# Performance work log

Measured on AMD Instinct MI355X. Metric: run time of the kernel, lower is better.

The kernel has to match this reference:

```python
import jax, jax.numpy as jnp
import numpy as np

BLOCK_SIZE = 256
N_EMBD = 256
HEAD_SIZE = 64


def setup_inputs() -> dict:
    key = jax.random.key(0)
    k1, k2, k3, k4, k5 = jax.random.split(key, 5)
    B, T = 256, 256
    x = jax.random.normal(k1, (B, T, N_EMBD), dtype=jnp.float32)
    # nn.Linear(n_embd, head_size, bias=False) weights, stored as [in, out] for x @ W
    s = 1.0 / np.sqrt(N_EMBD)
    Wk = jax.random.uniform(k2, (N_EMBD, HEAD_SIZE), minval=-s, maxval=s, dtype=jnp.float32)
    Wq = jax.random.uniform(k3, (N_EMBD, HEAD_SIZE), minval=-s, maxval=s, dtype=jnp.float32)
    Wv = jax.random.uniform(k4, (N_EMBD, HEAD_SIZE), minval=-s, maxval=s, dtype=jnp.float32)
    rel_pos_embedding = 0.02 * jax.random.normal(k5, (2 * BLOCK_SIZE - 1, HEAD_SIZE), dtype=jnp.float32)
    return {"x": x, "Wk": Wk, "Wq": Wq, "Wv": Wv, "rel_pos_embedding": rel_pos_embedding}


def reference(x, Wk, Wq, Wv, rel_pos_embedding):
    B, T, C = x.shape
    H = Wk.shape[-1]
    k = x @ Wk  # [B,T,H]
    q = x @ Wq  # [B,T,H]
    v = x @ Wv  # [B,T,H]
    # content scores (scaled); note: position scores are NOT scaled, matching original
    content = jnp.einsum('bth,bsh->bts', q, k) * (H ** -0.5)  # [B,T,T]
    # relative position indices: j - i + (block_size - 1)
    idx = jnp.arange(T)[None, :] - jnp.arange(T)[:, None] + (BLOCK_SIZE - 1)  # [T,T]
    rel_emb = rel_pos_embedding[idx]  # [T,T,H]
    position = jnp.einsum('bth,tsh->bts', q, rel_emb)  # [B,T,T]
    wei = content + position
    causal = jnp.tril(jnp.ones((T, T), dtype=bool))
    wei = jnp.where(causal[None, :, :], wei, -jnp.inf)
    wei = jax.nn.softmax(wei, axis=-1)
    # dropout omitted (eval mode / deterministic reference)
    out = jnp.einsum('bts,bsh->bth', wei, v)  # [B,T,H]
    return out
```

## Files before the change

kernel.cpp:

```cpp
#include <hip/hip_runtime.h>

#define BB 256
#define TT 256
#define CC 256
#define HH 64

typedef _Float16 half8 __attribute__((ext_vector_type(8)));
typedef _Float16 half4 __attribute__((ext_vector_type(4)));
typedef __fp16 fp16x2 __attribute__((ext_vector_type(2)));
typedef float floatx4 __attribute__((ext_vector_type(4)));

__global__ __launch_bounds__(256) void prep(
    const float* __restrict__ rpe,
    const float* __restrict__ Wk, const float* __restrict__ Wq, const float* __restrict__ Wv,
    _Float16* __restrict__ rpeh, _Float16* __restrict__ WT)
{
    const int bid = blockIdx.x, tid = threadIdx.x;
    if (bid < 64) {
        const int i = bid * 256 + tid;
        rpeh[i] = (_Float16)rpe[i];
    } else {
        const int wsel = (bid - 64) >> 6;
        const int n    = (bid - 64) & 63;
        const float* W = wsel == 0 ? Wk : (wsel == 1 ? Wq : Wv);
        WT[(size_t)(wsel * 64 + n) * 256 + tid] = (_Float16)W[tid * HH + n];
    }
}

__global__ __launch_bounds__(1024) void proj_mfma(
    const float* __restrict__ x, const _Float16* __restrict__ WT,
    _Float16* __restrict__ qh, _Float16* __restrict__ kh, _Float16* __restrict__ vTh)
{
    __shared__ _Float16 ws[192 * 256];
    const int tid = threadIdx.x;

#pragma unroll
    for (int i = tid; i < 192 * 32; i += 1024) {
        const int row = i >> 5;
        const int g   = i & 31;
        const int pg  = g ^ (row & 31);
        *(half8*)&ws[row * 256 + pg * 8] = *(const half8*)(WT + (size_t)row * 256 + g * 8);
    }
    __syncthreads();

    const int w    = tid >> 6;
    const int lane = tid & 63;
    const int quad = lane >> 4;
    const int l    = lane & 15;
    const int row0 = blockIdx.x * 256 + w * 16;

    floatx4 acc[12];
#pragma unroll
    for (int nt = 0; nt < 12; ++nt) acc[nt] = (floatx4){0.f, 0.f, 0.f, 0.f};

    const float4* xg = reinterpret_cast<const float4*>(x);
    union H8 { half8 v; fp16x2 p[4]; };

#pragma unroll
    for (int kk = 0; kk < 8; ++kk) {
        const size_t base = (size_t)(row0 + l) * 64 + kk * 8 + quad * 2;
        const float4 alo = xg[base], ahi = xg[base + 1];
        H8 u;
        u.p[0] = __builtin_amdgcn_cvt_pkrtz(alo.x, alo.y);
        u.p[1] = __builtin_amdgcn_cvt_pkrtz(alo.z, alo.w);
        u.p[2] = __builtin_amdgcn_cvt_pkrtz(ahi.x, ahi.y);
        u.p[3] = __builtin_amdgcn_cvt_pkrtz(ahi.z, ahi.w);

#pragma unroll
        for (int nt = 0; nt < 12; ++nt) {
            const int row = nt * 16 + l;
            const int pg  = (kk * 4 + quad) ^ (row & 31);
            const half8 bf = *(const half8*)&ws[row * 256 + pg * 8];
            acc[nt] = __builtin_amdgcn_mfma_f32_16x16x32_f16(u.v, bf, acc[nt], 0, 0, 0);
        }
    }

    const int bq  = blockIdx.x;
    const int trw = w * 16;
#pragma unroll
    for (int nt = 0; nt < 4; ++nt) {
#pragma unroll
        for (int r = 0; r < 4; ++r) {
            const size_t row = (size_t)row0 + quad * 4 + r;
            kh[row * HH + nt * 16 + l] = (_Float16)(acc[nt][r] * 0.125f);
            qh[row * HH + nt * 16 + l] = (_Float16)acc[nt + 4][r];
        }
        half4 vv;
        vv[0] = (_Float16)acc[nt + 8][0];
        vv[1] = (_Float16)acc[nt + 8][1];
        vv[2] = (_Float16)acc[nt + 8][2];
        vv[3] = (_Float16)acc[nt + 8][3];
        *(half4*)(vTh + ((size_t)bq * HH + nt * 16 + l) * TT + trw + quad * 4) = vv;
    }
}

__global__ __launch_bounds__(256) void flash(
    const _Float16* __restrict__ qh, const _Float16* __restrict__ kh,
    const _Float16* __restrict__ vTh, const _Float16* __restrict__ rpeh,
    float* __restrict__ out)
{
    __shared__ _Float16 weih[4][16 * 264];

    const int xcd  = blockIdx.x & 7;
    const int j    = blockIdx.x >> 3;
    const int b    = xcd * 32 + (j & 31);
    const int t0   = (j >> 5) * 64;
    const int w    = threadIdx.x >> 6;
    const int lane = threadIdx.x & 63;
    const int quad = lane >> 4;
    const int l    = lane & 15;
    const int tw   = t0 + 16 * w;
    const int stmax = tw >> 4;
    const int cmax  = (tw + 15) >> 5;
    const int dtmin = 15 - stmax;

    const _Float16* qp = qh + (size_t)(b * TT + tw + l) * HH + quad * 8;
    const half8 qf0 = *(const half8*)qp;
    const half8 qf1 = *(const half8*)(qp + 32);

#pragma unroll
    for (int dt = 0; dt < 16; ++dt) {
        if (dt >= dtmin) {
            const _Float16* rp = rpeh + (size_t)(dt * 16 + l) * HH + quad * 8;
            const half8 bf0 = *(const half8*)rp;
            const half8 bf1 = *(const half8*)(rp + 32);
            floatx4 z = {0.f, 0.f, 0.f, 0.f};
            z = __builtin_amdgcn_mfma_f32_16x16x32_f16(qf0, bf0, z, 0, 0, 0);
            const floatx4 pacc = __builtin_amdgcn_mfma_f32_16x16x32_f16(qf1, bf1, z, 0, 0, 0);
            if (dt == dtmin) {
#pragma unroll
                for (int r = 0; r < 4; ++r) {
                    const int row = quad * 4 + r;
                    const int s   = l + row - 15;
                    if (s >= 0) weih[w][row * 264 + s] = (_Float16)pacc[r];
                }
            } else {
#pragma unroll
                for (int r = 0; r < 4; ++r) {
                    const int row = quad * 4 + r;
                    const int s   = dt * 16 + l + tw + row - 255;
                    weih[w][row * 264 + s] = (_Float16)pacc[r];
                }
            }
        }
    }

    floatx4 sacc[16];
#pragma unroll
    for (int st = 0; st < 16; ++st) {
        if (st <= stmax) {
            const _Float16* kp = kh + (size_t)(b * TT + st * 16 + l) * HH + quad * 8;
            const half8 kf0 = *(const half8*)kp;
            const half8 kf1 = *(const half8*)(kp + 32);
            floatx4 z = {0.f, 0.f, 0.f, 0.f};
            z = __builtin_amdgcn_mfma_f32_16x16x32_f16(qf0, kf0, z, 0, 0, 0);
            sacc[st] = __builtin_amdgcn_mfma_f32_16x16x32_f16(qf1, kf1, z, 0, 0, 0);
        }
    }

    float sums[4] = {0.f, 0.f, 0.f, 0.f};
#pragma unroll
    for (int st = 0; st < 16; ++st) {
        if (st < stmax) {
            const int s = l + 16 * st;
#pragma unroll
            for (int r = 0; r < 4; ++r) {
                const int row = quad * 4 + r;
                const float e = __expf(sacc[st][r] + (float)weih[w][row * 264 + s]);
                sums[r] += e;
                weih[w][row * 264 + s] = (_Float16)e;
            }
        }
    }
    {
        const int s = l + 16 * stmax;
#pragma unroll
        for (int r = 0; r < 4; ++r) {
            const int row = quad * 4 + r;
            float e = 0.f;
            if (l <= row) e = __expf(sacc[stmax][r] + (float)weih[w][row * 264 + s]);
            sums[r] += e;
            weih[w][row * 264 + s] = (_Float16)e;
        }
    }
    if ((tw & 16) == 0) {
        const int s = l + 16 * (stmax + 1);
#pragma unroll
        for (int r = 0; r < 4; ++r) weih[w][(quad * 4 + r) * 264 + s] = (_Float16)0.f;
    }

    float inv_r[4];
#pragma unroll
    for (int r = 0; r < 4; ++r) {
        float sum = sums[r];
        sum += __shfl_xor(sum, 1);
        sum += __shfl_xor(sum, 2);
        sum += __shfl_xor(sum, 4);
        sum += __shfl_xor(sum, 8);
        inv_r[r] = 1.0f / sum;
    }

    floatx4 oacc[4] = {{0.f,0.f,0.f,0.f},{0.f,0.f,0.f,0.f},
                       {0.f,0.f,0.f,0.f},{0.f,0.f,0.f,0.f}};
#pragma unroll
    for (int c = 0; c < 8; ++c) {
        if (c <= cmax) {
            const half8 af = *(const half8*)&weih[w][l * 264 + c * 32 + quad * 8];
#pragma unroll
            for (int ht = 0; ht < 4; ++ht) {
                const half8 vf = *(const half8*)(vTh +
                    ((size_t)b * HH + ht * 16 + l) * TT + c * 32 + quad * 8);
                oacc[ht] = __builtin_amdgcn_mfma_f32_16x16x32_f16(af, vf, oacc[ht], 0, 0, 0);
            }
        }
    }

#pragma unroll
    for (int ht = 0; ht < 4; ++ht) {
#pragma unroll
        for (int r = 0; r < 4; ++r) {
            const int t = tw + quad * 4 + r;
            out[(size_t)(b * TT + t) * HH + ht * 16 + l] = oacc[ht][r] * inv_r[r];
        }
    }
}

extern "C" void kernel_launch(void* const* d_in, const int* in_sizes, int n_in,
                              void* d_out, int out_size, void* d_ws, size_t ws_size,
                              hipStream_t stream) {
    const float* x   = (const float*)d_in[0];
    const float* Wk  = (const float*)d_in[1];
    const float* Wq  = (const float*)d_in[2];
    const float* Wv  = (const float*)d_in[3];
    const float* rpe = (const float*)d_in[4];
    float* out = (float*)d_out;

    const size_t NQ = (size_t)BB * TT * HH;
    _Float16* qh   = (_Float16*)d_ws;
    _Float16* kh   = qh + NQ;
    _Float16* vTh  = kh + NQ;
    _Float16* rpeh = vTh + NQ;
    _Float16* WT   = rpeh + 256 * HH;

    prep<<<dim3(256), dim3(256), 0, stream>>>(rpe, Wk, Wq, Wv, rpeh, WT);
    proj_mfma<<<dim3(BB), dim3(1024), 0, stream>>>(x, WT, qh, kh, vTh);
    flash<<<dim3(BB * 4), dim3(256), 0, stream>>>(qh, kh, vTh, rpeh, out);
}
```

Measured before the change: 148.1 us.

## Fuse QKV projection and causal attention into one per-batch kernel

Merges the projection kernel and the attention kernel into a single kernel with one 1024-thread block per batch. The block first computes q, k and v^T into the workspace, synchronises, then each of its 16 waves runs the attention for one 16-row query tile, reusing the LDS buffer. This removes one kernel launch and the inter-kernel dependency, and keeps the freshly written q/k/v hot in cache. In exchange it drops from 1024 attention blocks to 256 with an imbalanced causal workload across waves, and it uses a large LDS allocation plus a launch-bounds occupancy hint that may constrain registers.

```diff
diff --git a/kernel.cpp b/kernel.cpp
--- a/kernel.cpp
+++ b/kernel.cpp
@@ -27,200 +27,195 @@
     }
 }
 
-__global__ __launch_bounds__(1024) void proj_mfma(
+__global__ __launch_bounds__(1024, 4) void fused(
     const float* __restrict__ x, const _Float16* __restrict__ WT,
-    _Float16* __restrict__ qh, _Float16* __restrict__ kh, _Float16* __restrict__ vTh)
+    const _Float16* __restrict__ rpeh,
+    _Float16* __restrict__ qh, _Float16* __restrict__ kh, _Float16* __restrict__ vTh,
+    float* __restrict__ out)
 {
-    __shared__ _Float16 ws[192 * 256];
-    const int tid = threadIdx.x;
+    __shared__ __align__(16) unsigned char ldsbuf[16 * 16 * 264 * 2];
+    _Float16* wt = (_Float16*)ldsbuf;
+
+    const int tid  = threadIdx.x;
+    const int b    = blockIdx.x;
+    const int w    = tid >> 6;
+    const int lane = tid & 63;
+    const int quad = lane >> 4;
+    const int l    = lane & 15;
+
+    union H8 { half8 v; fp16x2 p[4]; };
 
 #pragma unroll
     for (int i = tid; i < 192 * 32; i += 1024) {
         const int row = i >> 5;
         const int g   = i & 31;
         const int pg  = g ^ (row & 31);
-        *(half8*)&ws[row * 256 + pg * 8] = *(const half8*)(WT + (size_t)row * 256 + g * 8);
+        *(half8*)&wt[row * 256 + pg * 8] = *(const half8*)(WT + (size_t)row * 256 + g * 8);
     }
     __syncthreads();
 
-    const int w    = tid >> 6;
-    const int lane = tid & 63;
-    const int quad = lane >> 4;
-    const int l    = lane & 15;
-    const int row0 = blockIdx.x * 256 + w * 16;
-
-    floatx4 acc[12];
-#pragma unroll
-    for (int nt = 0; nt < 12; ++nt) acc[nt] = (floatx4){0.f, 0.f, 0.f, 0.f};
-
-    const float4* xg = reinterpret_cast<const float4*>(x);
-    union H8 { half8 v; fp16x2 p[4]; };
-
-#pragma unroll
-    for (int kk = 0; kk < 8; ++kk) {
-        const size_t base = (size_t)(row0 + l) * 64 + kk * 8 + quad * 2;
-        const float4 alo = xg[base], ahi = xg[base + 1];
-        H8 u;
-        u.p[0] = __builtin_amdgcn_cvt_pkrtz(alo.x, alo.y);
-        u.p[1] = __builtin_amdgcn_cvt_pkrtz(alo.z, alo.w);
-        u.p[2] = __builtin_amdgcn_cvt_pkrtz(ahi.x, ahi.y);
-        u.p[3] = __builtin_amdgcn_cvt_pkrtz(ahi.z, ahi.w);
-
-#pragma unroll
-        for (int nt = 0; nt < 12; ++nt) {
-            const int row = nt * 16 + l;
-            const int pg  = (kk * 4 + quad) ^ (row & 31);
-            const half8 bf = *(const half8*)&ws[row * 256 + pg * 8];
-            acc[nt] = __builtin_amdgcn_mfma_f32_16x16x32_f16(u.v, bf, acc[nt], 0, 0, 0);
-        }
-    }
-
-    const int bq  = blockIdx.x;
-    const int trw = w * 16;
-#pragma unroll
-    for (int nt = 0; nt < 4; ++nt) {
-#pragma unroll
-        for (int r = 0; r < 4; ++r) {
-            const size_t row = (size_t)row0 + quad * 4 + r;
-            kh[row * HH + nt * 16 + l] = (_Float16)(acc[nt][r] * 0.125f);
-            qh[row * HH + nt * 16 + l] = (_Float16)acc[nt + 4][r];
-        }
-        half4 vv;
-        vv[0] = (_Float16)acc[nt + 8][0];
-        vv[1] = (_Float16)acc[nt + 8][1];
-        vv[2] = (_Float16)acc[nt + 8][2];
-        vv[3] = (_Float16)acc[nt + 8][3];
-        *(half4*)(vTh + ((size_t)bq * HH + nt * 16 + l) * TT + trw + quad * 4) = vv;
-    }
-}
-
-__global__ __launch_bounds__(256) void flash(
-    const _Float16* __restrict__ qh, const _Float16* __restrict__ kh,
-    const _Float16* __restrict__ vTh, const _Float16* __restrict__ rpeh,
-    float* __restrict__ out)
-{
-    __shared__ _Float16 weih[4][16 * 264];
-
-    const int xcd  = blockIdx.x & 7;
-    const int j    = blockIdx.x >> 3;
-    const int b    = xcd * 32 + (j & 31);
-    const int t0   = (j >> 5) * 64;
-    const int w    = threadIdx.x >> 6;
-    const int lane = threadIdx.x & 63;
-    const int quad = lane >> 4;
-    const int l    = lane & 15;
-    const int tw   = t0 + 16 * w;
-    const int stmax = tw >> 4;
-    const int cmax  = (tw + 15) >> 5;
-    const int dtmin = 15 - stmax;
-
-    const _Float16* qp = qh + (size_t)(b * TT + tw + l) * HH + quad * 8;
-    const half8 qf0 = *(const half8*)qp;
-    const half8 qf1 = *(const half8*)(qp + 32);
-
-#pragma unroll
-    for (int dt = 0; dt < 16; ++dt) {
-        if (dt >= dtmin) {
-            const _Float16* rp = rpeh + (size_t)(dt * 16 + l) * HH + quad * 8;
-            const half8 bf0 = *(const half8*)rp;
-            const half8 bf1 = *(const half8*)(rp + 32);
-            floatx4 z = {0.f, 0.f, 0.f, 0.f};
-            z = __builtin_amdgcn_mfma_f32_16x16x32_f16(qf0, bf0, z, 0, 0, 0);
-            const floatx4 pacc = __builtin_amdgcn_mfma_f32_16x16x32_f16(qf1, bf1, z, 0, 0, 0);
-            if (dt == dtmin) {
+    {
+        const int row0 = b * 256 + w * 16;
+        floatx4 acc[12];
+#pragma unroll
+        for (int nt = 0; nt < 12; ++nt) acc[nt] = (floatx4){0.f, 0.f, 0.f, 0.f};
+
+        const float4* xg = reinterpret_cast<const float4*>(x);
+
+#pragma unroll
+        for (int kk = 0; kk < 8; ++kk) {
+            const size_t base = (size_t)(row0 + l) * 64 + kk * 8 + quad * 2;
+            const float4 alo = xg[base], ahi = xg[base + 1];
+            H8 u;
+            u.p[0] = __builtin_amdgcn_cvt_pkrtz(alo.x, alo.y);
+            u.p[1] = __builtin_amdgcn_cvt_pkrtz(alo.z, alo.w);
+            u.p[2] = __builtin_amdgcn_cvt_pkrtz(ahi.x, ahi.y);
+            u.p[3] = __builtin_amdgcn_cvt_pkrtz(ahi.z, ahi.w);
+
+#pragma unroll
+            for (int nt = 0; nt < 12; ++nt) {
+                const int row = nt * 16 + l;
+                const int pg  = (kk * 4 + quad) ^ (row & 31);
+                const half8 bf = *(const half8*)&wt[row * 256 + pg * 8];
+                acc[nt] = __builtin_amdgcn_mfma_f32_16x16x32_f16(u.v, bf, acc[nt], 0, 0, 0);
+            }
+        }
+
+        const int trw = w * 16;
+#pragma unroll
+        for (int nt = 0; nt < 4; ++nt) {
+#pragma unroll
+            for (int r = 0; r < 4; ++r) {
+                const size_t row = (size_t)row0 + quad * 4 + r;
+                kh[row * HH + nt * 16 + l] = (_Float16)(acc[nt][r] * 0.125f);
+                qh[row * HH + nt * 16 + l] = (_Float16)acc[nt + 4][r];
+            }
+            half4 vv;
+            vv[0] = (_Float16)acc[nt + 8][0];
+            vv[1] = (_Float16)acc[nt + 8][1];
+            vv[2] = (_Float16)acc[nt + 8][2];
+            vv[3] = (_Float16)acc[nt + 8][3];
+            *(half4*)(vTh + ((size_t)b * HH + nt * 16 + l) * TT + trw + quad * 4) = vv;
+        }
+    }
+    __syncthreads();
+
+    _Float16* wh = (_Float16*)ldsbuf + w * (16 * 264);
+    {
+        const int tile  = w;
+        const int tw    = tile * 16;
+        const int stmax = tile;
+        const int cmax  = tile >> 1;
+        const int dtmin = 15 - tile;
+
+        const _Float16* qp = qh + (size_t)(b * TT + tw + l) * HH + quad * 8;
+        const half8 qf0 = *(const half8*)qp;
+        const half8 qf1 = *(const half8*)(qp + 32);
+
+#pragma unroll
+        for (int dt = 0; dt < 16; ++dt) {
+            if (dt >= dtmin) {
+                const _Float16* rp = rpeh + (size_t)(dt * 16 + l) * HH + quad * 8;
+                const half8 bf0 = *(const half8*)rp;
+                const half8 bf1 = *(const half8*)(rp + 32);
+                floatx4 z = {0.f, 0.f, 0.f, 0.f};
+                z = __builtin_amdgcn_mfma_f32_16x16x32_f16(qf0, bf0, z, 0, 0, 0);
+                const floatx4 pacc = __builtin_amdgcn_mfma_f32_16x16x32_f16(qf1, bf1, z, 0, 0, 0);
+                if (dt == dtmin) {
+#pragma unroll
+                    for (int r = 0; r < 4; ++r) {
+                        const int row = quad * 4 + r;
+                        const int s   = l + row - 15;
+                        if (s >= 0) wh[row * 264 + s] = (_Float16)pacc[r];
+                    }
+                } else {
+#pragma unroll
+                    for (int r = 0; r < 4; ++r) {
+                        const int row = quad * 4 + r;
+                        const int s   = dt * 16 + l + tw + row - 255;
+                        wh[row * 264 + s] = (_Float16)pacc[r];
+                    }
+                }
+            }
+        }
+
+        floatx4 sacc[16];
+#pragma unroll
+        for (int st = 0; st < 16; ++st) {
+            if (st <= stmax) {
+                const _Float16* kp = kh + (size_t)(b * TT + st * 16 + l) * HH + quad * 8;
+                const half8 kf0 = *(const half8*)kp;
+                const half8 kf1 = *(const half8*)(kp + 32);
+                floatx4 z = {0.f, 0.f, 0.f, 0.f};
+                z = __builtin_amdgcn_mfma_f32_16x16x32_f16(qf0, kf0, z, 0, 0, 0);
+                sacc[st] = __builtin_amdgcn_mfma_f32_16x16x32_f16(qf1, kf1, z, 0, 0, 0);
+            }
+        }
+
+        float sums[4] = {0.f, 0.f, 0.f, 0.f};
+#pragma unroll
+        for (int st = 0; st < 16; ++st) {
+            if (st < stmax) {
+                const int s = l + 16 * st;
 #pragma unroll
                 for (int r = 0; r < 4; ++r) {
                     const int row = quad * 4 + r;
-                    const int s   = l + row - 15;
-                    if (s >= 0) weih[w][row * 264 + s] = (_Float16)pacc[r];
+                    const float e = __expf(sacc[st][r] + (float)wh[row * 264 + s]);
+                    sums[r] += e;
+                    wh[row * 264 + s] = (_Float16)e;
                 }
-            } else {
-#pragma unroll
-                for (int r = 0; r < 4; ++r) {
-                    const int row = quad * 4 + r;
-                    const int s   = dt * 16 + l + tw + row - 255;
-                    weih[w][row * 264 + s] = (_Float16)pacc[r];
-                }
-            }
-        }
-    }
-
-    floatx4 sacc[16];
-#pragma unroll
-    for (int st = 0; st < 16; ++st) {
-        if (st <= stmax) {
-            const _Float16* kp = kh + (size_t)(b * TT + st * 16 + l) * HH + quad * 8;
-            const half8 kf0 = *(const half8*)kp;
-            const half8 kf1 = *(const half8*)(kp + 32);
-            floatx4 z = {0.f, 0.f, 0.f, 0.f};
-            z = __builtin_amdgcn_mfma_f32_16x16x32_f16(qf0, kf0, z, 0, 0, 0);
-            sacc[st] = __builtin_amdgcn_mfma_f32_16x16x32_f16(qf1, kf1, z, 0, 0, 0);
-        }
-    }
-
-    float sums[4] = {0.f, 0.f, 0.f, 0.f};
-#pragma unroll
-    for (int st = 0; st < 16; ++st) {
-        if (st < stmax) {
-            const int s = l + 16 * st;
+            }
+        }
+        {
+            const int s = l + 16 * stmax;
 #pragma unroll
             for (int r = 0; r < 4; ++r) {
                 const int row = quad * 4 + r;
-                const float e = __expf(sacc[st][r] + (float)weih[w][row * 264 + s]);
+                float e = 0.f;
+                if (l <= row) e = __expf(sacc[stmax][r] + (float)wh[row * 264 + s]);
                 sums[r] += e;
-                weih[w][row * 264 + s] = (_Float16)e;
-            }
-        }
-    }
-    {
-        const int s = l + 16 * stmax;
+                wh[row * 264 + s] = (_Float16)e;
+            }
+        }
+        if ((tile & 1) == 0) {
+            const int s = l + 16 * (stmax + 1);
+#pragma unroll
+            for (int r = 0; r < 4; ++r) wh[(quad * 4 + r) * 264 + s] = (_Float16)0.f;
+        }
+
+        float inv_r[4];
 #pragma unroll
         for (int r = 0; r < 4; ++r) {
-            const int row = quad * 4 + r;
-            float e = 0.f;
-            if (l <= row) e = __expf(sacc[stmax][r] + (float)weih[w][row * 264 + s]);
-            sums[r] += e;
-            weih[w][row * 264 + s] = (_Float16)e;
-        }
-    }
-    if ((tw & 16) == 0) {
-        const int s = l + 16 * (stmax + 1);
-#pragma unroll
-        for (int r = 0; r < 4; ++r) weih[w][(quad * 4 + r) * 264 + s] = (_Float16)0.f;
-    }
-
-    float inv_r[4];
-#pragma unroll
-    for (int r = 0; r < 4; ++r) {
-        float sum = sums[r];
-        sum += __shfl_xor(sum, 1);
-        sum += __shfl_xor(sum, 2);
-        sum += __shfl_xor(sum, 4);
-        sum += __shfl_xor(sum, 8);
-        inv_r[r] = 1.0f / sum;
-    }
-
-    floatx4 oacc[4] = {{0.f,0.f,0.f,0.f},{0.f,0.f,0.f,0.f},
-                       {0.f,0.f,0.f,0.f},{0.f,0.f,0.f,0.f}};
-#pragma unroll
-    for (int c = 0; c < 8; ++c) {
-        if (c <= cmax) {
-            const half8 af = *(const half8*)&weih[w][l * 264 + c * 32 + quad * 8];
-#pragma unroll
-            for (int ht = 0; ht < 4; ++ht) {
-                const half8 vf = *(const half8*)(vTh +
-                    ((size_t)b * HH + ht * 16 + l) * TT + c * 32 + quad * 8);
-                oacc[ht] = __builtin_amdgcn_mfma_f32_16x16x32_f16(af, vf, oacc[ht], 0, 0, 0);
-            }
-        }
-    }
-
-#pragma unroll
-    for (int ht = 0; ht < 4; ++ht) {
-#pragma unroll
-        for (int r = 0; r < 4; ++r) {
-            const int t = tw + quad * 4 + r;
-            out[(size_t)(b * TT + t) * HH + ht * 16 + l] = oacc[ht][r] * inv_r[r];
+            float sum = sums[r];
+            sum += __shfl_xor(sum, 1);
+            sum += __shfl_xor(sum, 2);
+            sum += __shfl_xor(sum, 4);
+            sum += __shfl_xor(sum, 8);
+            inv_r[r] = 1.0f / sum;
+        }
+
+        floatx4 oacc[4] = {{0.f,0.f,0.f,0.f},{0.f,0.f,0.f,0.f},
+                           {0.f,0.f,0.f,0.f},{0.f,0.f,0.f,0.f}};
+#pragma unroll
+        for (int c = 0; c < 8; ++c) {
+            if (c <= cmax) {
+                const half8 af = *(const half8*)&wh[l * 264 + c * 32 + quad * 8];
+#pragma unroll
+                for (int ht = 0; ht < 4; ++ht) {
+                    const half8 vf = *(const half8*)(vTh +
+                        ((size_t)b * HH + ht * 16 + l) * TT + c * 32 + quad * 8);
+                    oacc[ht] = __builtin_amdgcn_mfma_f32_16x16x32_f16(af, vf, oacc[ht], 0, 0, 0);
+                }
+            }
+        }
+
+#pragma unroll
+        for (int ht = 0; ht < 4; ++ht) {
+#pragma unroll
+            for (int r = 0; r < 4; ++r) {
+                const int t = tw + quad * 4 + r;
+                out[(size_t)(b * TT + t) * HH + ht * 16 + l] = oacc[ht][r] * inv_r[r];
+            }
         }
     }
 }
@@ -243,6 +238,5 @@
     _Float16* WT   = rpeh + 256 * HH;
 
     prep<<<dim3(256), dim3(256), 0, stream>>>(rpe, Wk, Wq, Wv, rpeh, WT);
-    proj_mfma<<<dim3(BB), dim3(1024), 0, stream>>>(x, WT, qh, kh, vTh);
-    flash<<<dim3(BB * 4), dim3(256), 0, stream>>>(qh, kh, vTh, rpeh, out);
+    fused<<<dim3(BB), dim3(1024), 0, stream>>>(x, WT, rpeh, qh, kh, vTh, out);
 }
```

Result: no change. 146.0 us (-1.4%).
